# Kernel tuning notes

Hardware: AMD Instinct MI355X
Metric: run time of the kernel (lower is better)

Reference implementation:

```python
import jax, jax.numpy as jnp
import numpy as np

T, B, C, N, H = 4, 32, 384, 196, 12
D = C // H
HID = 1536
ALPHA = 4.0  # spikingjelly default sigmoid surrogate alpha
EPS = 1e-5   # BatchNorm eps
SCALE = 0.25

@jax.custom_vjp
def spike(x):
    return (x >= 0.0).astype(x.dtype)

def _spike_fwd(x):
    return (x >= 0.0).astype(x.dtype), x

def _spike_bwd(x, g):
    s = jax.nn.sigmoid(ALPHA * x)
    return (g * ALPHA * s * (1.0 - s),)

spike.defvjp(_spike_fwd, _spike_bwd)

def lif(x, thr=1.0, tau=2.0):
    # Multi-step LIF, hard reset to 0, detach_reset=True; x: (T, ...)
    def step(v, xt):
        v = v + (xt - v) / tau
        s = spike(v - thr)
        v = v * (1.0 - jax.lax.stop_gradient(s))
        return v, s
    _, out = jax.lax.scan(step, jnp.zeros_like(x[0]), x)
    return out

def conv_bn(x, w, b, g, beta, m, var):
    # 1x1 Conv1d (= channel matmul) + inference-form BatchNorm1d; x: (T,B,Cin,N), w: (Cout,Cin)
    y = jnp.einsum('tbcn,oc->tbon', x, w)
    if b is not None:
        y = y + b[:, None]
    inv = g * jax.lax.rsqrt(var + EPS)
    return y * inv[:, None] + (beta - m * inv)[:, None]

def _heads(t):
    # (T,B,C,N) -> (T,B,H,N,D), matching transpose(-1,-2).reshape(T,B,N,H,D).permute(0,1,3,2,4)
    return jnp.swapaxes(t, -1, -2).reshape(T, B, N, H, D).transpose(0, 1, 3, 2, 4)

def block_fwd(x, policy, wq, qg, qb, qm, qv, wk, kg, kb, km, kvv, wv, vg, vb, vm, vvv,
              wp, bp, pg, pb, pm, pv, w1, b1, g1, be1, m1, v1, w2, b2, g2, be2, m2, v2):
    q = _heads(lif(conv_bn(x, wq, None, qg, qb, qm, qv)))
    k = _heads(lif(conv_bn(x, wk, None, kg, kb, km, kvv)))
    v = _heads(lif(conv_bn(x, wv, None, vg, vb, vm, vvv)))
    attn = jnp.einsum('tbhnd,tbhmd->tbhnm', q, k)           # (T,B,H,N,N)
    pr = policy.reshape(T, B, 1, 1, N)
    eye = jnp.eye(N, dtype=x.dtype)
    attn = attn * (pr + (1.0 - pr) * eye)                   # attention_policy masking
    o = jnp.einsum('tbhnm,tbhmd->tbhnd', attn, v) * SCALE
    o = jnp.swapaxes(o, 3, 4).reshape(T, B, C, N)           # transpose(3,4).reshape(T,B,C,N)
    o = lif(o, thr=0.5)                                     # attn_lif v_threshold=0.5
    o = lif(conv_bn(o, wp, bp, pg, pb, pm, pv))             # proj conv+bn+lif
    x = x + o                                               # residual 1
    h = lif(conv_bn(x, w1, b1, g1, be1, m1, v1))            # MLP fc1
    h = lif(conv_bn(h, w2, b2, g2, be2, m2, v2))            # MLP fc2
    return x + h                                            # residual 2

def setup_inputs():
    key = jax.random.key(0)
    ks = iter(jax.random.split(key, 48))
    def nrm(shape, s=1.0):
        return jax.random.normal(next(ks), shape, jnp.float32) * s
    def uni(shape):
        return jax.random.uniform(next(ks), shape, jnp.float32, minval=0.5, maxval=1.5)
    inp = {}
    inp['x'] = nrm((T, B, C, N))
    inp['policy'] = (jax.random.uniform(next(ks), (T * B, N, 1)) > 0.3).astype(jnp.float32)
    inp.update({'wq': nrm((C, C), 0.05), 'qg': jnp.ones((C,)), 'qb': jnp.zeros((C,)), 'qm': nrm((C,), 0.1), 'qv': uni((C,))})
    inp.update({'wk': nrm((C, C), 0.05), 'kg': jnp.ones((C,)), 'kb': jnp.zeros((C,)), 'km': nrm((C,), 0.1), 'kvv': uni((C,))})
    inp.update({'wv': nrm((C, C), 0.05), 'vg': jnp.ones((C,)), 'vb': jnp.zeros((C,)), 'vm': nrm((C,), 0.1), 'vvv': uni((C,))})
    inp.update({'wp': nrm((C, C), 0.05), 'bp': jnp.zeros((C,)), 'pg': jnp.ones((C,)), 'pb': jnp.zeros((C,)), 'pm': nrm((C,), 0.1), 'pv': uni((C,))})
    inp.update({'w1': nrm((HID, C), 0.05), 'b1': jnp.zeros((HID,)), 'g1': jnp.ones((HID,)), 'be1': jnp.zeros((HID,)), 'm1': nrm((HID,), 0.1), 'v1': uni((HID,))})
    inp.update({'w2': nrm((C, HID), 0.05), 'b2': jnp.zeros((C,)), 'g2': jnp.ones((C,)), 'be2': jnp.zeros((C,)), 'm2': nrm((C,), 0.1), 'v2': uni((C,))})
    return inp

def reference(x, policy, wq, qg, qb, qm, qv, wk, kg, kb, km, kvv, wv, vg, vb, vm, vvv,
              wp, bp, pg, pb, pm, pv, w1, b1, g1, be1, m1, v1, w2, b2, g2, be2, m2, v2):
    return block_fwd(x, policy, wq, qg, qb, qm, qv, wk, kg, kb, km, kvv, wv, vg, vb, vm, vvv,
                     wp, bp, pg, pb, pm, pv, w1, b1, g1, be1, m1, v1, w2, b2, g2, be2, m2, v2)
```

## Files before the change

kernel.cpp:

```cpp
#include <hip/hip_runtime.h>
#include <cstdint>
#include <cstddef>

#define N_POS 196

typedef __attribute__((ext_vector_type(4))) float f32x4;

__device__ __forceinline__ void async_copy16(const float* g, float* l) {
    __builtin_amdgcn_global_load_lds(
        (const __attribute__((address_space(1))) uint32_t*)g,
        (__attribute__((address_space(3))) uint32_t*)l,
        16, 0, 0);
}

template<int CIN, bool USE_FMA, bool ACCUM>
__global__ __launch_bounds__(256, 4) void convbn_kernel(
    const float* __restrict__ X, const float* __restrict__ W,
    const float* __restrict__ Bi, const float* __restrict__ Ga,
    const float* __restrict__ Be, const float* __restrict__ Mu,
    const float* __restrict__ Va, float* __restrict__ Y, int Cout,
    int nb, int b0, int xlocal, int ylocal)
{
#pragma clang fp contract(off)
    constexpr int NCH = CIN / 16;
    __shared__ float lds[2 * 3136 + 2 * 1024];
    float* Xs = lds;
    float* Ws = lds + 6272;
    const int tid = threadIdx.x;
    const int l   = blockIdx.x;
    const int t   = l / nb;
    const int bl  = l - t * nb;
    const int tbg = t * 32 + b0 + bl;
    const int xtb = xlocal ? l : tbg;
    const int ytb = ylocal ? l : tbg;
    const int o0  = blockIdx.y * 64;
    const int o   = tid & 31;
    const int grp = tid >> 5;
    const float* Xtb = X + (size_t)xtb * CIN * N_POS;
    const float* Wp  = W + (size_t)o0 * CIN;

    f32x4 accA[8], accB[8];
    #pragma unroll
    for (int i = 0; i < 8; ++i) { accA[i] = (f32x4)0.f; accB[i] = (f32x4)0.f; }

    auto stage = [&](int buf, int kc) {
        const int oo = tid >> 2, k4 = tid & 3;
        float4 wv4 = *(const float4*)(Wp + (size_t)oo * CIN + kc + k4 * 4);
        #pragma unroll
        for (int j = 0; j < 4; ++j) {
            int i = tid + j * 256;
            if (i < 784)
                async_copy16(Xtb + (size_t)(kc + i / 49) * N_POS + (i % 49) * 4,
                             &Xs[buf * 3136 + (i & ~63) * 4]);
        }
        Ws[buf * 1024 + (k4 * 4 + 0) * 64 + oo] = wv4.x;
        Ws[buf * 1024 + (k4 * 4 + 1) * 64 + oo] = wv4.y;
        Ws[buf * 1024 + (k4 * 4 + 2) * 64 + oo] = wv4.z;
        Ws[buf * 1024 + (k4 * 4 + 3) * 64 + oo] = wv4.w;
    };

    stage(0, 0);
    __syncthreads();
    int buf = 0;
    for (int ch = 0; ch < NCH; ++ch) {
        if (ch + 1 < NCH) stage(buf ^ 1, (ch + 1) * 16);
        const float* Xb = Xs + buf * 3136 + o * 4;
        const float* Wb = Ws + buf * 1024 + grp * 8;
        #pragma unroll
        for (int kk = 0; kk < 16; ++kk) {
            f32x4 xA = *(const f32x4*)(Xb + kk * 196);
            f32x4 xB = *(const f32x4*)(Xb + kk * 196 + 128);
            float4 wA = *(const float4*)(Wb + kk * 64);
            float4 wB = *(const float4*)(Wb + kk * 64 + 4);
            float w8[8] = { wA.x, wA.y, wA.z, wA.w, wB.x, wB.y, wB.z, wB.w };
            #pragma unroll
            for (int i = 0; i < 8; ++i) {
                f32x4 wd = { w8[i], w8[i], w8[i], w8[i] };
                if (USE_FMA) {
                    accA[i] = __builtin_elementwise_fma(wd, xA, accA[i]);
                    accB[i] = __builtin_elementwise_fma(wd, xB, accB[i]);
                } else {
                    accA[i] = accA[i] + wd * xA;
                    accB[i] = accB[i] + wd * xB;
                }
            }
        }
        __syncthreads();
        buf ^= 1;
    }

    #pragma unroll
    for (int i = 0; i < 8; ++i) {
        int oo = o0 + grp * 8 + i;
        float sc = __fmul_rn(Ga[oo], 1.0f / sqrtf(__fadd_rn(Va[oo], 1e-5f)));
        float sh = __fsub_rn(Be[oo], __fmul_rn(Mu[oo], sc));
        float bi = Bi ? Bi[oo] : 0.f;
        float* yp = Y + ((size_t)ytb * Cout + oo) * N_POS;
        {
            float a[4] = { accA[i].x, accA[i].y, accA[i].z, accA[i].w };
            float4 r;
            float* rp = &r.x;
            #pragma unroll
            for (int j = 0; j < 4; ++j) {
                float y = Bi ? __fadd_rn(a[j], bi) : a[j];
                rp[j] = __fadd_rn(__fmul_rn(y, sc), sh);
            }
            float* dst = yp + o * 4;
            if (ACCUM) {
                float4 y0 = *(const float4*)dst;
                r.x = __fadd_rn(y0.x, r.x); r.y = __fadd_rn(y0.y, r.y);
                r.z = __fadd_rn(y0.z, r.z); r.w = __fadd_rn(y0.w, r.w);
            }
            *(float4*)dst = r;
        }
        if (o <= 16) {
            float a[4] = { accB[i].x, accB[i].y, accB[i].z, accB[i].w };
            float4 r;
            float* rp = &r.x;
            #pragma unroll
            for (int j = 0; j < 4; ++j) {
                float y = Bi ? __fadd_rn(a[j], bi) : a[j];
                rp[j] = __fadd_rn(__fmul_rn(y, sc), sh);
            }
            float* dst = yp + 128 + o * 4;
            if (ACCUM) {
                float4 y0 = *(const float4*)dst;
                r.x = __fadd_rn(y0.x, r.x); r.y = __fadd_rn(y0.y, r.y);
                r.z = __fadd_rn(y0.z, r.z); r.w = __fadd_rn(y0.w, r.w);
            }
            *(float4*)dst = r;
        }
    }
}

__global__ __launch_bounds__(256) void lif_kernel(float* __restrict__ Y, int plane4, float thr)
{
    int idx = blockIdx.x * 256 + threadIdx.x;
    if (idx >= plane4) return;
    float4* Yp = (float4*)Y;
    float v0 = 0.f, v1 = 0.f, v2 = 0.f, v3 = 0.f;
    #pragma unroll
    for (int t = 0; t < 4; ++t) {
        float4 xv = Yp[(size_t)t * plane4 + idx];
        v0 = __fadd_rn(v0, __fmul_rn(__fsub_rn(xv.x, v0), 0.5f));
        v1 = __fadd_rn(v1, __fmul_rn(__fsub_rn(xv.y, v1), 0.5f));
        v2 = __fadd_rn(v2, __fmul_rn(__fsub_rn(xv.z, v2), 0.5f));
        v3 = __fadd_rn(v3, __fmul_rn(__fsub_rn(xv.w, v3), 0.5f));
        float s0 = (__fsub_rn(v0, thr) >= 0.f) ? 1.f : 0.f;
        float s1 = (__fsub_rn(v1, thr) >= 0.f) ? 1.f : 0.f;
        float s2 = (__fsub_rn(v2, thr) >= 0.f) ? 1.f : 0.f;
        float s3 = (__fsub_rn(v3, thr) >= 0.f) ? 1.f : 0.f;
        v0 = __fmul_rn(v0, 1.f - s0); v1 = __fmul_rn(v1, 1.f - s1);
        v2 = __fmul_rn(v2, 1.f - s2); v3 = __fmul_rn(v3, 1.f - s3);
        xv.x = s0; xv.y = s1; xv.z = s2; xv.w = s3;
        Yp[(size_t)t * plane4 + idx] = xv;
    }
}

__global__ __launch_bounds__(256) void lif_add_kernel(
    const float* __restrict__ Yin, float* __restrict__ Out, int b0)
{
    const int PL4 = 8 * 384 * 49;
    const int B4  = 384 * 49;
    int idx = blockIdx.x * 256 + threadIdx.x;
    if (idx >= PL4) return;
    int bl = idx / B4, r = idx - bl * B4;
    const float4* Yp = (const float4*)Yin;
    float v0 = 0.f, v1 = 0.f, v2 = 0.f, v3 = 0.f;
    #pragma unroll
    for (int t = 0; t < 4; ++t) {
        float4 xv = Yp[(size_t)t * PL4 + idx];
        v0 = __fadd_rn(v0, __fmul_rn(__fsub_rn(xv.x, v0), 0.5f));
        v1 = __fadd_rn(v1, __fmul_rn(__fsub_rn(xv.y, v1), 0.5f));
        v2 = __fadd_rn(v2, __fmul_rn(__fsub_rn(xv.z, v2), 0.5f));
        v3 = __fadd_rn(v3, __fmul_rn(__fsub_rn(xv.w, v3), 0.5f));
        float s0 = (__fsub_rn(v0, 1.0f) >= 0.f) ? 1.f : 0.f;
        float s1 = (__fsub_rn(v1, 1.0f) >= 0.f) ? 1.f : 0.f;
        float s2 = (__fsub_rn(v2, 1.0f) >= 0.f) ? 1.f : 0.f;
        float s3 = (__fsub_rn(v3, 1.0f) >= 0.f) ? 1.f : 0.f;
        v0 = __fmul_rn(v0, 1.f - s0); v1 = __fmul_rn(v1, 1.f - s1);
        v2 = __fmul_rn(v2, 1.f - s2); v3 = __fmul_rn(v3, 1.f - s3);
        float4* op = (float4*)Out + ((size_t)(t * 32 + b0 + bl) * B4 + r);
        float4 o = *op;
        o.x = __fadd_rn(o.x, s0); o.y = __fadd_rn(o.y, s1);
        o.z = __fadd_rn(o.z, s2); o.w = __fadd_rn(o.w, s3);
        *op = o;
    }
}

__global__ __launch_bounds__(256) void pack_kernel(const float* __restrict__ S,
                                                   uint32_t* __restrict__ Bits)
{
    int idx = blockIdx.x * 256 + threadIdx.x;
    if (idx >= 4 * 32 * 12 * 196) return;
    int n = idx % 196;
    int rest = idx / 196;
    int h = rest % 12;
    int tb = rest / 12;
    const float* sp = S + ((size_t)tb * 384 + h * 32) * 196 + n;
    uint32_t bits = 0;
    #pragma unroll
    for (int d = 0; d < 32; ++d)
        bits |= (sp[(size_t)d * 196] > 0.5f) ? (1u << d) : 0u;
    Bits[idx] = bits;
}

__global__ __launch_bounds__(256) void attn_kernel(
    const uint32_t* __restrict__ Qb, const uint32_t* __restrict__ Kb,
    const float* __restrict__ V, const float* __restrict__ P, float* __restrict__ O)
{
    __shared__ uint32_t Qbs[196], Kbs[196];
    __shared__ float Ps[196];
    __shared__ float Vs[32][204];
    __shared__ float Ss[32][204];
    __shared__ float Os[32][36];
    const int tid = threadIdx.x;
    const int bid = blockIdx.x;
    const int tb = bid / 12, h = bid - tb * 12;
    const size_t vbase = ((size_t)tb * 384 + h * 32) * 196;
    const size_t qbase = ((size_t)tb * 12 + h) * 196;
    for (int i = tid; i < 196; i += 256) {
        Qbs[i] = Qb[qbase + i];
        Kbs[i] = Kb[qbase + i];
        Ps[i]  = P[(size_t)tb * 196 + i];
    }
    for (int i = tid; i < 32 * 49; i += 256) {
        int d = i / 49, m4 = i - d * 49;
        *(float4*)&Vs[d][m4 * 4] = *(const float4*)(V + vbase + (size_t)d * 196 + m4 * 4);
    }
    __syncthreads();
    for (int n0 = 0; n0 < 196; n0 += 32) {
        const int rows = min(32, 196 - n0);
        for (int idx = tid; idx < rows * 196; idx += 256) {
            int ns = idx / 196, m = idx - ns * 196;
            int n = n0 + ns;
            float s = (float)__popc(Qbs[n] & Kbs[m]);
            float p = Ps[m];
            float e = (m == n) ? 1.f : 0.f;
            Ss[ns][m] = s * (p + (1.f - p) * e);
        }
        __syncthreads();
        {
            const int tn = tid & 15, td = tid >> 4;
            float a00 = 0, a01 = 0, a10 = 0, a11 = 0;
            #pragma unroll 7
            for (int m4 = 0; m4 < 49; ++m4) {
                float4 s0 = *(const float4*)&Ss[tn][m4 * 4];
                float4 s1 = *(const float4*)&Ss[tn + 16][m4 * 4];
                float4 u0 = *(const float4*)&Vs[td][m4 * 4];
                float4 u1 = *(const float4*)&Vs[td + 16][m4 * 4];
                a00 += s0.x * u0.x + s0.y * u0.y + s0.z * u0.z + s0.w * u0.w;
                a01 += s0.x * u1.x + s0.y * u1.y + s0.z * u1.z + s0.w * u1.w;
                a10 += s1.x * u0.x + s1.y * u0.y + s1.z * u0.z + s1.w * u0.w;
                a11 += s1.x * u1.x + s1.y * u1.y + s1.z * u1.z + s1.w * u1.w;
            }
            Os[td     ][tn     ] = a00 * 0.25f;
            Os[td + 16][tn     ] = a01 * 0.25f;
            Os[td     ][tn + 16] = a10 * 0.25f;
            Os[td + 16][tn + 16] = a11 * 0.25f;
        }
        __syncthreads();
        {
            const int d = tid >> 3, c4 = tid & 7;
            if (c4 * 4 < rows)
                *(float4*)(O + vbase + (size_t)d * 196 + n0 + c4 * 4) =
                    *(const float4*)&Os[d][c4 * 4];
        }
        __syncthreads();
    }
}

__global__ __launch_bounds__(256) void add_kernel(const float* __restrict__ A,
    const float* __restrict__ B, float* __restrict__ Out, int n4)
{
    int idx = blockIdx.x * 256 + threadIdx.x;
    if (idx >= n4) return;
    float4 a = ((const float4*)A)[idx];
    float4 b = ((const float4*)B)[idx];
    float4 o;
    o.x = __fadd_rn(a.x, b.x); o.y = __fadd_rn(a.y, b.y);
    o.z = __fadd_rn(a.z, b.z); o.w = __fadd_rn(a.w, b.w);
    ((float4*)Out)[idx] = o;
}

extern "C" void kernel_launch(void* const* d_in, const int* in_sizes, int n_in,
                              void* d_out, int out_size, void* d_ws, size_t ws_size,
                              hipStream_t stream) {
    const float* x   = (const float*)d_in[0];
    const float* pol = (const float*)d_in[1];
    const float* wq = (const float*)d_in[2];
    const float* qg = (const float*)d_in[3];
    const float* qb = (const float*)d_in[4];
    const float* qm = (const float*)d_in[5];
    const float* qv = (const float*)d_in[6];
    const float* wk = (const float*)d_in[7];
    const float* kg = (const float*)d_in[8];
    const float* kb = (const float*)d_in[9];
    const float* km = (const float*)d_in[10];
    const float* kvv= (const float*)d_in[11];
    const float* wv = (const float*)d_in[12];
    const float* vg = (const float*)d_in[13];
    const float* vb = (const float*)d_in[14];
    const float* vm = (const float*)d_in[15];
    const float* vvv= (const float*)d_in[16];
    const float* wp = (const float*)d_in[17];
    const float* bp = (const float*)d_in[18];
    const float* pg = (const float*)d_in[19];
    const float* pb = (const float*)d_in[20];
    const float* pm = (const float*)d_in[21];
    const float* pv = (const float*)d_in[22];
    const float* w1 = (const float*)d_in[23];
    const float* b1 = (const float*)d_in[24];
    const float* g1 = (const float*)d_in[25];
    const float* be1= (const float*)d_in[26];
    const float* m1 = (const float*)d_in[27];
    const float* v1 = (const float*)d_in[28];
    const float* w2 = (const float*)d_in[29];
    const float* b2 = (const float*)d_in[30];
    const float* g2 = (const float*)d_in[31];
    const float* be2= (const float*)d_in[32];
    const float* m2 = (const float*)d_in[33];
    const float* v2 = (const float*)d_in[34];

    float* bufA = (float*)d_ws;
    float* bufD = bufA + 9633792;
    uint32_t* Qbits = (uint32_t*)(bufD + 2408448);
    uint32_t* Kbits = Qbits + 301056;
    float* out = (float*)d_out;

    convbn_kernel<384, false, false><<<dim3(128, 6), 256, 0, stream>>>(x, wq, nullptr, qg, qb, qm, qv, bufA, 384, 32, 0, 0, 0);
    lif_kernel<<<2352, 256, 0, stream>>>(bufA, 602112, 1.0f);
    pack_kernel<<<1176, 256, 0, stream>>>(bufA, Qbits);
    convbn_kernel<384, false, false><<<dim3(128, 6), 256, 0, stream>>>(x, wk, nullptr, kg, kb, km, kvv, bufA, 384, 32, 0, 0, 0);
    lif_kernel<<<2352, 256, 0, stream>>>(bufA, 602112, 1.0f);
    pack_kernel<<<1176, 256, 0, stream>>>(bufA, Kbits);
    convbn_kernel<384, false, false><<<dim3(128, 6), 256, 0, stream>>>(x, wv, nullptr, vg, vb, vm, vvv, bufA, 384, 32, 0, 0, 0);
    lif_kernel<<<2352, 256, 0, stream>>>(bufA, 602112, 1.0f);

    attn_kernel<<<1536, 256, 0, stream>>>(Qbits, Kbits, bufA, pol, out);
    lif_kernel<<<2352, 256, 0, stream>>>(out, 602112, 0.5f);

    convbn_kernel<384, true, false><<<dim3(128, 6), 256, 0, stream>>>(out, wp, bp, pg, pb, pm, pv, bufA, 384, 32, 0, 0, 0);
    lif_kernel<<<2352, 256, 0, stream>>>(bufA, 602112, 1.0f);
    add_kernel<<<9408, 256, 0, stream>>>(x, bufA, out, 2408448);

    for (int c = 0; c < 4; ++c) {
        convbn_kernel<384, false, false><<<dim3(32, 24), 256, 0, stream>>>(out, w1, b1, g1, be1, m1, v1, bufA, 1536, 8, c * 8, 0, 1);
        lif_kernel<<<2352, 256, 0, stream>>>(bufA, 602112, 1.0f);
        convbn_kernel<1536, true, false><<<dim3(32, 6), 256, 0, stream>>>(bufA, w2, b2, g2, be2, m2, v2, bufD, 384, 8, c * 8, 1, 1);
        lif_add_kernel<<<588, 256, 0, stream>>>(bufD, out, c * 8);
    }
}
```

Before: 2.411 ms.

## Load transposed weights directly into registers and drop weight LDS staging

```diff
diff --git a/kernel.cpp b/kernel.cpp
--- a/kernel.cpp
+++ b/kernel.cpp
@@ -13,9 +13,28 @@
         16, 0, 0);
 }
 
-template<int CIN, bool USE_FMA, bool ACCUM>
-__global__ __launch_bounds__(256, 4) void convbn_kernel(
-    const float* __restrict__ X, const float* __restrict__ W,
+__global__ __launch_bounds__(256) void transpose_kernel(
+    const float* __restrict__ A, float* __restrict__ At, int R, int C)
+{
+    __shared__ float tile[32][33];
+    const int c0 = blockIdx.x * 32, r0 = blockIdx.y * 32;
+    const int tx = threadIdx.x & 31, ty = threadIdx.x >> 5;
+    #pragma unroll
+    for (int dy = 0; dy < 32; dy += 8) {
+        int r = r0 + ty + dy, c = c0 + tx;
+        if (r < R && c < C) tile[ty + dy][tx] = A[(size_t)r * C + c];
+    }
+    __syncthreads();
+    #pragma unroll
+    for (int dy = 0; dy < 32; dy += 8) {
+        int c = c0 + ty + dy, r = r0 + tx;
+        if (c < C && r < R) At[(size_t)c * R + r] = tile[tx][ty + dy];
+    }
+}
+
+template<int CIN, int OPT, bool USE_FMA, bool ACCUM>
+__global__ __launch_bounds__(256) void convbn_kernel(
+    const float* __restrict__ X, const float* __restrict__ WT,
     const float* __restrict__ Bi, const float* __restrict__ Ga,
     const float* __restrict__ Be, const float* __restrict__ Mu,
     const float* __restrict__ Va, float* __restrict__ Y, int Cout,
@@ -23,9 +42,9 @@
 {
 #pragma clang fp contract(off)
     constexpr int NCH = CIN / 16;
-    __shared__ float lds[2 * 3136 + 2 * 1024];
-    float* Xs = lds;
-    float* Ws = lds + 6272;
+    constexpr int NG  = NCH * 4;
+    constexpr int NF4 = OPT / 4;
+    __shared__ float Xs[2 * 3136 + 64];
     const int tid = threadIdx.x;
     const int l   = blockIdx.x;
     const int t   = l / nb;
@@ -33,19 +52,30 @@
     const int tbg = t * 32 + b0 + bl;
     const int xtb = xlocal ? l : tbg;
     const int ytb = ylocal ? l : tbg;
-    const int o0  = blockIdx.y * 64;
+    const int o0  = blockIdx.y * (8 * OPT);
     const int o   = tid & 31;
     const int grp = tid >> 5;
+    const int obase = o0 + grp * OPT;
     const float* Xtb = X + (size_t)xtb * CIN * N_POS;
-    const float* Wp  = W + (size_t)o0 * CIN;
-
-    f32x4 accA[8], accB[8];
-    #pragma unroll
-    for (int i = 0; i < 8; ++i) { accA[i] = (f32x4)0.f; accB[i] = (f32x4)0.f; }
+    const float* WTb = WT + obase;
+
+    f32x4 accA[OPT], accB[OPT];
+    #pragma unroll
+    for (int i = 0; i < OPT; ++i) { accA[i] = (f32x4)0.f; accB[i] = (f32x4)0.f; }
+
+    f32x4 wbufA[4 * NF4], wbufB[4 * NF4];
+
+    auto loadW = [&](f32x4* wb, int kg) {
+        const int kbase = kg * 4;
+        #pragma unroll
+        for (int kk = 0; kk < 4; ++kk)
+            #pragma unroll
+            for (int f = 0; f < NF4; ++f)
+                wb[kk * NF4 + f] =
+                    *(const f32x4*)(WTb + (size_t)(kbase + kk) * Cout + f * 4);
+    };
 
     auto stage = [&](int buf, int kc) {
-        const int oo = tid >> 2, k4 = tid & 3;
-        float4 wv4 = *(const float4*)(Wp + (size_t)oo * CIN + kc + k4 * 4);
         #pragma unroll
         for (int j = 0; j < 4; ++j) {
             int i = tid + j * 256;
@@ -53,29 +83,18 @@
                 async_copy16(Xtb + (size_t)(kc + i / 49) * N_POS + (i % 49) * 4,
                              &Xs[buf * 3136 + (i & ~63) * 4]);
         }
-        Ws[buf * 1024 + (k4 * 4 + 0) * 64 + oo] = wv4.x;
-        Ws[buf * 1024 + (k4 * 4 + 1) * 64 + oo] = wv4.y;
-        Ws[buf * 1024 + (k4 * 4 + 2) * 64 + oo] = wv4.z;
-        Ws[buf * 1024 + (k4 * 4 + 3) * 64 + oo] = wv4.w;
     };
 
-    stage(0, 0);
-    __syncthreads();
-    int buf = 0;
-    for (int ch = 0; ch < NCH; ++ch) {
-        if (ch + 1 < NCH) stage(buf ^ 1, (ch + 1) * 16);
-        const float* Xb = Xs + buf * 3136 + o * 4;
-        const float* Wb = Ws + buf * 1024 + grp * 8;
+    auto compute = [&](const f32x4* wb, int buf, int g) {
+        const float* Xb = Xs + buf * 3136 + ((g & 3) * 4) * 196 + o * 4;
         #pragma unroll
-        for (int kk = 0; kk < 16; ++kk) {
+        for (int kk = 0; kk < 4; ++kk) {
             f32x4 xA = *(const f32x4*)(Xb + kk * 196);
             f32x4 xB = *(const f32x4*)(Xb + kk * 196 + 128);
-            float4 wA = *(const float4*)(Wb + kk * 64);
-            float4 wB = *(const float4*)(Wb + kk * 64 + 4);
-            float w8[8] = { wA.x, wA.y, wA.z, wA.w, wB.x, wB.y, wB.z, wB.w };
             #pragma unroll
-            for (int i = 0; i < 8; ++i) {
-                f32x4 wd = { w8[i], w8[i], w8[i], w8[i] };
+            for (int i = 0; i < OPT; ++i) {
+                float w = ((const float*)&wb[kk * NF4])[i];
+                f32x4 wd = { w, w, w, w };
                 if (USE_FMA) {
                     accA[i] = __builtin_elementwise_fma(wd, xA, accA[i]);
                     accB[i] = __builtin_elementwise_fma(wd, xB, accB[i]);
@@ -85,21 +104,32 @@
                 }
             }
         }
-        __syncthreads();
-        buf ^= 1;
-    }
-
-    #pragma unroll
-    for (int i = 0; i < 8; ++i) {
-        int oo = o0 + grp * 8 + i;
+    };
+
+    stage(0, 0);
+    loadW(wbufA, 0);
+    __syncthreads();
+    int buf = 0;
+    for (int gp = 0; gp < NG; gp += 2) {
+        if ((gp & 3) == 0 && (gp >> 2) + 1 < NCH)
+            stage(buf ^ 1, ((gp >> 2) + 1) * 16);
+        if (gp + 1 < NG) loadW(wbufB, gp + 1);
+        compute(wbufA, buf, gp);
+        if (gp + 2 < NG) loadW(wbufA, gp + 2);
+        compute(wbufB, buf, gp + 1);
+        if (((gp + 1) & 3) == 3) { __syncthreads(); buf ^= 1; }
+    }
+
+    #pragma unroll
+    for (int i = 0; i < OPT; ++i) {
+        int oo = obase + i;
         float sc = __fmul_rn(Ga[oo], 1.0f / sqrtf(__fadd_rn(Va[oo], 1e-5f)));
         float sh = __fsub_rn(Be[oo], __fmul_rn(Mu[oo], sc));
         float bi = Bi ? Bi[oo] : 0.f;
         float* yp = Y + ((size_t)ytb * Cout + oo) * N_POS;
         {
             float a[4] = { accA[i].x, accA[i].y, accA[i].z, accA[i].w };
-            float4 r;
-            float* rp = &r.x;
+            float4 r; float* rp = &r.x;
             #pragma unroll
             for (int j = 0; j < 4; ++j) {
                 float y = Bi ? __fadd_rn(a[j], bi) : a[j];
@@ -115,8 +145,7 @@
         }
         if (o <= 16) {
             float a[4] = { accB[i].x, accB[i].y, accB[i].z, accB[i].w };
-            float4 r;
-            float* rp = &r.x;
+            float4 r; float* rp = &r.x;
             #pragma unroll
             for (int j = 0; j < 4; ++j) {
                 float y = Bi ? __fadd_rn(a[j], bi) : a[j];
@@ -326,28 +355,41 @@
     float* bufD = bufA + 9633792;
     uint32_t* Qbits = (uint32_t*)(bufD + 2408448);
     uint32_t* Kbits = Qbits + 301056;
+    float* wqT = (float*)(Kbits + 301056);
+    float* wkT = wqT + 147456;
+    float* wvT = wkT + 147456;
+    float* wpT = wvT + 147456;
+    float* w1T = wpT + 147456;
+    float* w2T = w1T + 589824;
     float* out = (float*)d_out;
 
-    convbn_kernel<384, false, false><<<dim3(128, 6), 256, 0, stream>>>(x, wq, nullptr, qg, qb, qm, qv, bufA, 384, 32, 0, 0, 0);
+    transpose_kernel<<<dim3(12, 12), 256, 0, stream>>>(wq, wqT, 384, 384);
+    transpose_kernel<<<dim3(12, 12), 256, 0, stream>>>(wk, wkT, 384, 384);
+    transpose_kernel<<<dim3(12, 12), 256, 0, stream>>>(wv, wvT, 384, 384);
+    transpose_kernel<<<dim3(12, 12), 256, 0, stream>>>(wp, wpT, 384, 384);
+    transpose_kernel<<<dim3(12, 48), 256, 0, stream>>>(w1, w1T, 1536, 384);
+    transpose_kernel<<<dim3(48, 12), 256, 0, stream>>>(w2, w2T, 384, 1536);
+
+    convbn_kernel<384, 8, false, false><<<dim3(128, 6), 256, 0, stream>>>(x, wqT, nullptr, qg, qb, qm, qv, bufA, 384, 32, 0, 0, 0);
     lif_kernel<<<2352, 256, 0, stream>>>(bufA, 602112, 1.0f);
     pack_kernel<<<1176, 256, 0, stream>>>(bufA, Qbits);
-    convbn_kernel<384, false, false><<<dim3(128, 6), 256, 0, stream>>>(x, wk, nullptr, kg, kb, km, kvv, bufA, 384, 32, 0, 0, 0);
+    convbn_kernel<384, 8, false, false><<<dim3(128, 6), 256, 0, stream>>>(x, wkT, nullptr, kg, kb, km, kvv, bufA, 384, 32, 0, 0, 0);
     lif_kernel<<<2352, 256, 0, stream>>>(bufA, 602112, 1.0f);
     pack_kernel<<<1176, 256, 0, stream>>>(bufA, Kbits);
-    convbn_kernel<384, false, false><<<dim3(128, 6), 256, 0, stream>>>(x, wv, nullptr, vg, vb, vm, vvv, bufA, 384, 32, 0, 0, 0);
+    convbn_kernel<384, 8, false, false><<<dim3(128, 6), 256, 0, stream>>>(x, wvT, nullptr, vg, vb, vm, vvv, bufA, 384, 32, 0, 0, 0);
     lif_kernel<<<2352, 256, 0, stream>>>(bufA, 602112, 1.0f);
 
     attn_kernel<<<1536, 256, 0, stream>>>(Qbits, Kbits, bufA, pol, out);
     lif_kernel<<<2352, 256, 0, stream>>>(out, 602112, 0.5f);
 
-    convbn_kernel<384, true, false><<<dim3(128, 6), 256, 0, stream>>>(out, wp, bp, pg, pb, pm, pv, bufA, 384, 32, 0, 0, 0);
+    convbn_kernel<384, 8, true, false><<<dim3(128, 6), 256, 0, stream>>>(out, wpT, bp, pg, pb, pm, pv, bufA, 384, 32, 0, 0, 0);
     lif_kernel<<<2352, 256, 0, stream>>>(bufA, 602112, 1.0f);
     add_kernel<<<9408, 256, 0, stream>>>(x, bufA, out, 2408448);
 
     for (int c = 0; c < 4; ++c) {
-        convbn_kernel<384, false, false><<<dim3(32, 24), 256, 0, stream>>>(out, w1, b1, g1, be1, m1, v1, bufA, 1536, 8, c * 8, 0, 1);
+        convbn_kernel<384, 8, false, false><<<dim3(32, 24), 256, 0, stream>>>(out, w1T, b1, g1, be1, m1, v1, bufA, 1536, 8, c * 8, 0, 1);
         lif_kernel<<<2352, 256, 0, stream>>>(bufA, 602112, 1.0f);
-        convbn_kernel<1536, true, false><<<dim3(32, 6), 256, 0, stream>>>(bufA, w2, b2, g2, be2, m2, v2, bufD, 384, 8, c * 8, 1, 1);
+        convbn_kernel<1536, 4, true, false><<<dim3(32, 12), 256, 0, stream>>>(bufA, w2T, b2, g2, be2, m2, v2, bufD, 384, 8, c * 8, 1, 1);
         lif_add_kernel<<<588, 256, 0, stream>>>(bufD, out, c * 8);
     }
 }
```

Measured after the change: 3.128 ms. 1.3x slower.
